# Performance work log

Measured on AMD Instinct MI355X. Metric: run time of the kernel, lower is better.

## Reference

```python
import jax, jax.numpy as jnp
import numpy as np

SINKHORN_ALPHA = 0.05
OT_MAX_ITER = 100
STOP_THR = 0.005
EPS = 1e-16
N_TOPICS, VOCAB, DIM = 1024, 50000, 256


def setup_inputs() -> dict:
    key = jax.random.key(0)
    k1, k2 = jax.random.split(key)
    x = jax.random.uniform(k1, (N_TOPICS, DIM), dtype=jnp.float32)
    y = jax.random.uniform(k2, (VOCAB, DIM), dtype=jnp.float32)
    return {"x": x, "y": y}


def _pairwise_sq_euclidean(x, y):
    return (jnp.sum(x * x, axis=1, keepdims=True)
            + jnp.sum(y * y, axis=1)
            - 2.0 * (x @ y.T))


def reference(x, y):
    M = _pairwise_sq_euclidean(x, y)          # [n, m]
    n, m = M.shape
    dt = M.dtype
    a = jnp.full((n, 1), 1.0 / n, dtype=dt)    # uniform source marginal
    b = jnp.full((m, 1), 1.0 / m, dtype=dt)    # uniform target marginal
    K = jnp.exp(-M * SINKHORN_ALPHA)           # Gibbs kernel [n, m]
    u0 = jnp.full((n, 1), 1.0 / n, dtype=dt)
    v0 = jnp.zeros((m, 1), dtype=dt)

    def cond_fn(carry):
        u, v, err, cpt = carry
        return (err > STOP_THR) & (cpt < OT_MAX_ITER)

    def body_fn(carry):
        u, v, err, cpt = carry
        v = b / (K.T @ u + EPS)                # [m, 1]
        u = a / (K @ v + EPS)                  # [n, 1]
        cpt = cpt + 1

        def compute_err(_):
            bb = v * (K.T @ u)                 # current column marginal
            return jnp.max(jnp.sum(jnp.abs(bb - b), axis=0))

        # original: convergence check only when cpt % 50 == 1
        err = jax.lax.cond((cpt % 50) == 1, compute_err, lambda _: err, operand=None)
        return (u, v, err, cpt)

    init = (u0, v0, jnp.asarray(1.0, dt), jnp.asarray(0, jnp.int32))
    u, v, err, cpt = jax.lax.while_loop(cond_fn, body_fn, init)

    transp = u * (K * v.T)                     # transport plan [n, m]
    loss_etp = jnp.sum(transp * M)
    return (loss_etp, transp)
```

## Files before the change

kernel.cpp:

```cpp
#include <hip/hip_runtime.h>
#include <hip/hip_cooperative_groups.h>
#include <cstdint>

namespace cg = cooperative_groups;

#define N_T 1024
#define M_V 50000
#define DIMS 256
#define NPAD 50048
#define GPANELS 391
#define CBLK 196
#define NPART (CBLK * 64)
#define NCHUNK 782
#define J8TOT 6250
#define F8BLK 25
#define LPART (F8BLK * 64)

constexpr float ALPHA     = 0.05f;
constexpr float INV_ALPHA = 20.0f;
constexpr float A_VAL     = 1.0f / 1024.0f;
constexpr float B_VAL     = 1.0f / 50000.0f;
constexpr float THR       = 0.005f;
constexpr float EPSV      = 1e-16f;

typedef short    bf16x8 __attribute__((ext_vector_type(8)));
typedef float    f32x4  __attribute__((ext_vector_type(4)));
typedef _Float16 half8v __attribute__((ext_vector_type(8)));

__device__ __forceinline__ float blockReduce256(float val) {
  #pragma unroll
  for (int off = 32; off; off >>= 1) val += __shfl_down(val, off, 64);
  __shared__ float redw[4];
  int lane = threadIdx.x & 63;
  int wid  = threadIdx.x >> 6;
  if (lane == 0) redw[wid] = val;
  __syncthreads();
  float r = 0.0f;
  if (threadIdx.x == 0) r = redw[0] + redw[1] + redw[2] + redw[3];
  __syncthreads();
  return r;
}

__device__ __forceinline__ unsigned short f2bf(float f) {
  union { float f; unsigned u; } c{f};
  unsigned r = c.u + 0x7FFF + ((c.u >> 16) & 1);
  return (unsigned short)(r >> 16);
}
__device__ __forceinline__ float bf2f(unsigned short b) {
  union { unsigned u; float f; } c{(unsigned)b << 16};
  return c.f;
}

__device__ __forceinline__ void gload16(const void* g, void* l) {
  __builtin_amdgcn_global_load_lds((const __attribute__((address_space(1))) unsigned int*)g,
                                   (__attribute__((address_space(3))) unsigned int*)l, 16, 0, 0);
}

__global__ __launch_bounds__(256) void pack_kernel(const float* __restrict__ x,
                                                   const float* __restrict__ y,
                                                   unsigned short* __restrict__ Ap,
                                                   unsigned short* __restrict__ Bp,
                                                   float* __restrict__ xx,
                                                   float* __restrict__ yy) {
  __shared__ float rr[4];
  int lane = threadIdx.x & 63, wid = threadIdx.x >> 6;
  if (blockIdx.x < N_T / 2) {
    int r = blockIdx.x * 2 + (threadIdx.x >> 7);
    int k = (threadIdx.x & 127) * 2;
    float2 vx = *(const float2*)&x[(size_t)r * DIMS + k];
    ushort2 h2, l2;
    h2.x = f2bf(vx.x); h2.y = f2bf(vx.y);
    l2.x = f2bf(vx.x - bf2f(h2.x)); l2.y = f2bf(vx.y - bf2f(h2.y));
    *(ushort2*)&Ap[(size_t)r * 512 + k]       = h2;
    *(ushort2*)&Ap[(size_t)r * 512 + 256 + k] = l2;
    float ssq = vx.x * vx.x + vx.y * vx.y;
    #pragma unroll
    for (int off = 32; off; off >>= 1) ssq += __shfl_down(ssq, off, 64);
    if (lane == 0) rr[wid] = ssq;
    __syncthreads();
    if ((threadIdx.x & 127) == 0) xx[r] = rr[wid] + rr[wid + 1];
  } else {
    int r = (blockIdx.x - N_T / 2) * 2 + (threadIdx.x >> 7);
    int k = (threadIdx.x & 127) * 2;
    ushort2 h2 = {0, 0};
    float ssq = 0.0f;
    if (r < M_V) {
      float2 vy = *(const float2*)&y[(size_t)r * DIMS + k];
      h2.x = f2bf(vy.x); h2.y = f2bf(vy.y);
      ssq = vy.x * vy.x + vy.y * vy.y;
    }
    *(ushort2*)&Bp[(size_t)r * 256 + k] = h2;
    #pragma unroll
    for (int off = 32; off; off >>= 1) ssq += __shfl_down(ssq, off, 64);
    if (lane == 0) rr[wid] = ssq;
    __syncthreads();
    if ((threadIdx.x & 127) == 0 && r < M_V) yy[r] = rr[wid] + rr[wid + 1];
  }
}

__global__ __launch_bounds__(256) void mfma_gemm_kernel(const unsigned short* __restrict__ Ap,
                                                        const unsigned short* __restrict__ Bp,
                                                        const float* __restrict__ xx,
                                                        const float* __restrict__ yy,
                                                        _Float16* __restrict__ Kh,
                                                        float* __restrict__ colsumPart) {
  const int t  = blockIdx.x & 63;
  const int gb = blockIdx.x >> 6;
  const int panel = gb * 8 + (t & 7);
  const int rt    = t >> 3;
  if (panel >= GPANELS) return;
  const int i0 = rt * 128;
  const int j0 = panel * 128;

  __shared__ unsigned short Ah[2][128][32];
  __shared__ unsigned short Al[2][128][32];
  __shared__ unsigned short Bs[2][128][32];
  const int tid  = threadIdx.x;
  const int lane = tid & 63;
  const int wid  = tid >> 6;
  const int wr = wid >> 1, wc = wid & 1;

  f32x4 acc[4][4];
  #pragma unroll
  for (int m = 0; m < 4; ++m)
    #pragma unroll
    for (int n = 0; n < 4; ++n) acc[m][n] = (f32x4){0.f, 0.f, 0.f, 0.f};

  const int srow  = lane >> 2;
  const int sslot = lane & 3;

  auto STAGE = [&](int b, int k0) {
    #pragma unroll
    for (int q = 0; q < 2; ++q) {
      int rbase = (wid * 2 + q) * 16;
      int row = rbase + srow;
      int cg_ = sslot ^ ((row >> 1) & 3);
      gload16(Ap + (size_t)(i0 + row) * 512 + k0 + cg_ * 8,       &Ah[b][rbase][0]);
      gload16(Ap + (size_t)(i0 + row) * 512 + 256 + k0 + cg_ * 8, &Al[b][rbase][0]);
      gload16(Bp + (size_t)(j0 + row) * 256 + k0 + cg_ * 8,       &Bs[b][rbase][0]);
    }
  };

  STAGE(0, 0);
  int cur = 0;
  #pragma unroll
  for (int step = 0; step < 8; ++step) {
    if (step < 7) {
      STAGE(cur ^ 1, (step + 1) * 32);
      asm volatile("s_waitcnt vmcnt(6)" ::: "memory");
    } else {
      asm volatile("s_waitcnt vmcnt(0)" ::: "memory");
    }
    __builtin_amdgcn_s_barrier();
    __builtin_amdgcn_sched_barrier(0);
    bf16x8 ah[4], al[4], bb[4];
    #pragma unroll
    for (int m = 0; m < 4; ++m) {
      int row = wr * 64 + m * 16 + (lane & 15);
      int sl  = (lane >> 4) ^ ((row >> 1) & 3);
      ah[m] = *(const bf16x8*)&Ah[cur][row][sl * 8];
      al[m] = *(const bf16x8*)&Al[cur][row][sl * 8];
    }
    #pragma unroll
    for (int n = 0; n < 4; ++n) {
      int col = wc * 64 + n * 16 + (lane & 15);
      int sl  = (lane >> 4) ^ ((col >> 1) & 3);
      bb[n] = *(const bf16x8*)&Bs[cur][col][sl * 8];
    }
    #pragma unroll
    for (int m = 0; m < 4; ++m)
      #pragma unroll
      for (int n = 0; n < 4; ++n) {
        acc[m][n] = __builtin_amdgcn_mfma_f32_16x16x32_bf16(ah[m], bb[n], acc[m][n], 0, 0, 0);
        acc[m][n] = __builtin_amdgcn_mfma_f32_16x16x32_bf16(al[m], bb[n], acc[m][n], 0, 0, 0);
      }
    asm volatile("s_waitcnt lgkmcnt(0)" ::: "memory");
    __builtin_amdgcn_sched_barrier(0);
    __builtin_amdgcn_s_barrier();
    cur ^= 1;
  }

  float csum[4] = {0.f, 0.f, 0.f, 0.f};
  #pragma unroll
  for (int m = 0; m < 4; ++m) {
    int rowb = i0 + wr * 64 + m * 16 + (lane >> 4) * 4;
    #pragma unroll
    for (int n = 0; n < 4; ++n) {
      int col = j0 + wc * 64 + n * 16 + (lane & 15);
      float yyc = (col < M_V) ? yy[col] : 0.0f;
      #pragma unroll
      for (int r = 0; r < 4; ++r) {
        float mval = xx[rowb + r] + yyc - 2.0f * acc[m][n][r];
        _Float16 kh = (_Float16)__expf(-ALPHA * mval);
        if (col < M_V) Kh[(size_t)(rowb + r) * M_V + col] = kh;
        csum[n] += (float)kh;
      }
    }
  }
  #pragma unroll
  for (int n = 0; n < 4; ++n) {
    float c = csum[n];
    c += __shfl_xor(c, 16, 64);
    c += __shfl_xor(c, 32, 64);
    if (lane < 16) {
      int col = j0 + wc * 64 + n * 16 + lane;
      colsumPart[(size_t)(rt * 2 + wr) * NPAD + col] = c;
    }
  }
}

__global__ __launch_bounds__(256) void v1_kernel(const float* __restrict__ cp,
                                                 float* __restrict__ v,
                                                 float* __restrict__ errAcc,
                                                 int* __restrict__ counter) {
  int j = blockIdx.x * 256 + threadIdx.x;
  if (j == 0) { errAcc[0] = 0.0f; *counter = 0; }
  if (j < M_V) {
    float s = 0.0f;
    #pragma unroll
    for (int q = 0; q < 16; ++q) s += cp[(size_t)q * NPAD + j];
    v[j] = B_VAL / (s * A_VAL + EPSV);
  }
}

__global__ __launch_bounds__(256) void rowpass_kernel(const _Float16* __restrict__ Kh,
                                                      const float* __restrict__ v,
                                                      float* __restrict__ rowPart) {
  const int i = blockIdx.y;
  const int c = blockIdx.x;
  const half8v* K8 = (const half8v*)(Kh + (size_t)i * M_V);
  const float4* v4 = (const float4*)v;
  float p = 0.0f;
  int q = c * 3125 + threadIdx.x;
  #pragma unroll
  for (int it = 0; it < 12; ++it, q += 256) {
    half8v k8 = K8[q];
    float4 va = v4[q * 2], vb = v4[q * 2 + 1];
    p += (float)k8[0] * va.x + (float)k8[1] * va.y + (float)k8[2] * va.z + (float)k8[3] * va.w
       + (float)k8[4] * vb.x + (float)k8[5] * vb.y + (float)k8[6] * vb.z + (float)k8[7] * vb.w;
  }
  if (threadIdx.x < 53) {
    int q2 = c * 3125 + 3072 + threadIdx.x;
    half8v k8 = K8[q2];
    float4 va = v4[q2 * 2], vb = v4[q2 * 2 + 1];
    p += (float)k8[0] * va.x + (float)k8[1] * va.y + (float)k8[2] * va.z + (float)k8[3] * va.w
       + (float)k8[4] * vb.x + (float)k8[5] * vb.y + (float)k8[6] * vb.z + (float)k8[7] * vb.w;
  }
  p = blockReduce256(p);
  if (threadIdx.x == 0) rowPart[c * N_T + i] = p;
}

__global__ void u_kernel(const float* __restrict__ rowPart, float* __restrict__ u) {
  int i = blockIdx.x * 256 + threadIdx.x;
  u[i] = A_VAL / (rowPart[i] + rowPart[N_T + i] + EPSV);
}

__global__ __launch_bounds__(256) void specfinal_kernel(const _Float16* __restrict__ Kh,
                                                        const float* __restrict__ u_,
                                                        const float* __restrict__ v_,
                                                        float* __restrict__ out,
                                                        float* __restrict__ sPart,
                                                        float* __restrict__ lossPart) {
  const int j8 = blockIdx.x * 256 + threadIdx.x;
  const int by = blockIdx.y;
  float contrib = 0.0f;
  if (j8 < J8TOT) {
    const size_t jb = (size_t)j8 * 8;
    float4 va = ((const float4*)v_)[j8 * 2];
    float4 vb = ((const float4*)v_)[j8 * 2 + 1];
    float sp0 = 0.f, sp1 = 0.f, sp2 = 0.f, sp3 = 0.f;
    float sp4 = 0.f, sp5 = 0.f, sp6 = 0.f, sp7 = 0.f;
    #pragma unroll
    for (int r = 0; r < 16; ++r) {
      int i = by * 16 + r;
      half8v k8 = *(const half8v*)(Kh + (size_t)i * M_V + jb);
      float ui = u_[i];
      float k0 = (float)k8[0], k1 = (float)k8[1], k2 = (float)k8[2], k3 = (float)k8[3];
      float k4 = (float)k8[4], k5 = (float)k8[5], k6 = (float)k8[6], k7 = (float)k8[7];
      float t0 = ui * k0 * va.x, t1 = ui * k1 * va.y, t2 = ui * k2 * va.z, t3 = ui * k3 * va.w;
      float t4 = ui * k4 * vb.x, t5 = ui * k5 * vb.y, t6 = ui * k6 * vb.z, t7 = ui * k7 * vb.w;
      size_t o = 1 + (size_t)i * M_V + jb;
      out[o]     = t0; out[o + 1] = t1; out[o + 2] = t2; out[o + 3] = t3;
      out[o + 4] = t4; out[o + 5] = t5; out[o + 6] = t6; out[o + 7] = t7;
      contrib += t0 * (-__logf(k0)) + t1 * (-__logf(k1)) + t2 * (-__logf(k2)) + t3 * (-__logf(k3))
               + t4 * (-__logf(k4)) + t5 * (-__logf(k5)) + t6 * (-__logf(k6)) + t7 * (-__logf(k7));
      sp0 += k0 * ui; sp1 += k1 * ui; sp2 += k2 * ui; sp3 += k3 * ui;
      sp4 += k4 * ui; sp5 += k5 * ui; sp6 += k6 * ui; sp7 += k7 * ui;
    }
    float* sb = sPart + (size_t)by * M_V + jb;
    *(float4*)sb       = make_float4(sp0, sp1, sp2, sp3);
    *(float4*)(sb + 4) = make_float4(sp4, sp5, sp6, sp7);
  }
  contrib = blockReduce256(contrib) * INV_ALPHA;
  if (threadIdx.x == 0) lossPart[by * F8BLK + blockIdx.x] = contrib;
}

__global__ __launch_bounds__(256) void tail_kernel(const float* __restrict__ sPart,
                                                   const float* __restrict__ v_,
                                                   const float* __restrict__ lossPart,
                                                   float* errAcc, int* counter,
                                                   float* out, int* notconv) {
  int j = blockIdx.x * 256 + threadIdx.x;
  float e = 0.0f;
  if (j < M_V) {
    float ss = 0.0f;
    #pragma unroll
    for (int q = 0; q < 64; ++q) ss += sPart[(size_t)q * M_V + j];
    e = fabsf(v_[j] * ss - B_VAL);
  }
  e = blockReduce256(e);
  __shared__ int lastFlag;
  if (threadIdx.x == 0) {
    atomicAdd(errAcc, e);
    __threadfence();
    int old = atomicAdd(counter, 1);
    lastFlag = (old == (int)gridDim.x - 1) ? 1 : 0;
  }
  __syncthreads();
  if (lastFlag) {
    float ls = 0.0f;
    for (int i = threadIdx.x; i < LPART; i += 256) ls += lossPart[i];
    ls = blockReduce256(ls);
    if (threadIdx.x == 0) {
      out[0] = ls;
      *notconv = (errAcc[0] > THR) ? 1 : 0;
    }
  }
}

__global__ void set1_kernel(int* p) { *p = 1; }

template <typename KT>
__global__ __launch_bounds__(256, 4) void sinkhorn_coop(const KT* Km,
                                                        float* __restrict__ u,
                                                        float* __restrict__ v,
                                                        float* __restrict__ s,
                                                        float* __restrict__ errAcc,
                                                        const int* __restrict__ notconv) {
  if (*notconv == 0) return;
  cg::grid_group grid = cg::this_grid();
  __shared__ float su[N_T];
  __shared__ float red[8][64];
  const int tid = threadIdx.x;
  const int bid = blockIdx.x;
  const int nb  = gridDim.x;
  {
    int g0 = bid * 256 + tid;
    if (g0 < N_T) u[g0] = A_VAL;
    if (g0 < 2) errAcc[g0] = 0.0f;
  }
  grid.sync();
  for (int t = 1; t <= 100; ++t) {
    const bool check = (t == 2) || (t == 52);
    for (int i = tid; i < N_T; i += 256) su[i] = u[i];
    __syncthreads();
    const int g = tid >> 5, jl = tid & 31;
    float eacc = 0.0f;
    for (int c = bid; c < NCHUNK; c += nb) {
      const int j0 = c * 64;
      const int jj = j0 + jl * 2;
      float p0 = 0.f, p1 = 0.f;
      if (jj < M_V) {
        const KT* base = Km + (size_t)(g * 128) * M_V + jj;
        #pragma unroll 4
        for (int i = 0; i < 128; ++i) {
          float k0 = (float)base[(size_t)i * M_V];
          float k1 = (float)base[(size_t)i * M_V + 1];
          float uu = su[g * 128 + i];
          p0 += k0 * uu; p1 += k1 * uu;
        }
      }
      red[g][jl * 2]     = p0;
      red[g][jl * 2 + 1] = p1;
      __syncthreads();
      if (tid < 64) {
        int j = j0 + tid;
        if (j < M_V) {
          float st = 0.f;
          #pragma unroll
          for (int q = 0; q < 8; ++q) st += red[q][tid];
          if (check) {
            s[j] = st;
            eacc += fabsf(v[j] * st - B_VAL);
          } else {
            v[j] = B_VAL / (st + EPSV);
          }
        }
      }
      __syncthreads();
    }
    if (check) {
      float e = blockReduce256(eacc);
      if (tid == 0) atomicAdd(&errAcc[t == 2 ? 0 : 1], e);
    }
    grid.sync();
    if (check) {
      float e = errAcc[t == 2 ? 0 : 1];
      if (e <= THR) break;
      if (tid < 64) {
        for (int c = bid; c < NCHUNK; c += nb) {
          int j = c * 64 + tid;
          if (j < M_V) v[j] = B_VAL / (s[j] + EPSV);
        }
      }
      grid.sync();
    }
    for (int i = bid; i < N_T; i += nb) {
      float p = 0.f;
      const KT* row = Km + (size_t)i * M_V;
      for (int j = tid; j < M_V; j += 256) p += (float)row[j] * v[j];
      p = blockReduce256(p);
      if (tid == 0) u[i] = A_VAL / (p + EPSV);
    }
    grid.sync();
  }
}

template <typename KT>
__global__ __launch_bounds__(256) void final_kernel(const KT* Kmat,
                                                    const float* __restrict__ u,
                                                    const float* __restrict__ v,
                                                    float* out,
                                                    float* __restrict__ partials,
                                                    const int* __restrict__ gate) {
  if (*gate == 0) return;
  int j = blockIdx.x * 256 + threadIdx.x;
  float contrib = 0.0f;
  if (j < M_V) {
    float vj = v[j];
    #pragma unroll 4
    for (int r = 0; r < 16; ++r) {
      int i = blockIdx.y * 16 + r;
      size_t idx = (size_t)i * M_V + j;
      float k = (float)Kmat[idx];
      float tr = u[i] * k * vj;
      float m = -__logf(k) * INV_ALPHA;
      out[1 + idx] = tr;
      contrib += tr * m;
    }
  }
  contrib = blockReduce256(contrib);
  if (threadIdx.x == 0) partials[blockIdx.y * gridDim.x + blockIdx.x] = contrib;
}

__global__ __launch_bounds__(256) void finish_kernel(const float* __restrict__ partials,
                                                     float* out, int np_,
                                                     const int* __restrict__ gate) {
  if (*gate == 0) return;
  float s = 0.0f;
  for (int i = threadIdx.x; i < np_; i += 256) s += partials[i];
  s = blockReduce256(s);
  if (threadIdx.x == 0) out[0] = s;
}

__global__ __launch_bounds__(256) void sumsq_kernel(const float* __restrict__ in,
                                                    float* __restrict__ o, int rows) {
  int r = blockIdx.x;
  if (r >= rows) return;
  float v = in[(size_t)r * DIMS + threadIdx.x];
  float s = blockReduce256(v * v);
  if (threadIdx.x == 0) o[r] = s;
}

#define BM 64
#define BN 64
#define BK 32
__global__ __launch_bounds__(256) void gemm_k_kernel(const float* __restrict__ x,
                                                     const float* __restrict__ y,
                                                     const float* __restrict__ xx,
                                                     const float* __restrict__ yy,
                                                     float* Kmat) {
  __shared__ float As[BK][BM];
  __shared__ float Bs[BK][BN + 1];
  int tid = threadIdx.x;
  int i0 = blockIdx.y * BM;
  int j0 = blockIdx.x * BN;
  int tx = tid & 15, ty = tid >> 4;
  float acc[4][4] = {};
  for (int k0 = 0; k0 < DIMS; k0 += BK) {
    #pragma unroll
    for (int l = tid; l < 512; l += 256) {
      int r = l >> 3, kq = l & 7;
      float4 a4 = *(const float4*)&x[(size_t)(i0 + r) * DIMS + k0 + kq * 4];
      As[kq * 4 + 0][r] = a4.x; As[kq * 4 + 1][r] = a4.y;
      As[kq * 4 + 2][r] = a4.z; As[kq * 4 + 3][r] = a4.w;
    }
    #pragma unroll
    for (int l = tid; l < 512; l += 256) {
      int r = l >> 3, kq = l & 7;
      int j = j0 + r;
      float4 b4 = make_float4(0.f, 0.f, 0.f, 0.f);
      if (j < M_V) b4 = *(const float4*)&y[(size_t)j * DIMS + k0 + kq * 4];
      Bs[kq * 4 + 0][r] = b4.x; Bs[kq * 4 + 1][r] = b4.y;
      Bs[kq * 4 + 2][r] = b4.z; Bs[kq * 4 + 3][r] = b4.w;
    }
    __syncthreads();
    #pragma unroll
    for (int k = 0; k < BK; ++k) {
      float a[4], b[4];
      #pragma unroll
      for (int r = 0; r < 4; ++r) a[r] = As[k][ty * 4 + r];
      #pragma unroll
      for (int c = 0; c < 4; ++c) b[c] = Bs[k][tx * 4 + c];
      #pragma unroll
      for (int r = 0; r < 4; ++r)
        #pragma unroll
        for (int c = 0; c < 4; ++c) acc[r][c] += a[r] * b[c];
    }
    __syncthreads();
  }
  #pragma unroll
  for (int r = 0; r < 4; ++r) {
    int i = i0 + ty * 4 + r;
    float xxi = xx[i];
    #pragma unroll
    for (int c = 0; c < 4; ++c) {
      int j = j0 + tx * 4 + c;
      if (j < M_V) {
        float m = xxi + yy[j] - 2.0f * acc[r][c];
        Kmat[(size_t)i * M_V + j] = __expf(-ALPHA * m);
      }
    }
  }
}

extern "C" void kernel_launch(void* const* d_in, const int* in_sizes, int n_in,
                              void* d_out, int out_size, void* d_ws, size_t ws_size,
                              hipStream_t stream) {
  const float* x = (const float*)d_in[0];
  const float* y = (const float*)d_in[1];
  float* out = (float*)d_out;

  uintptr_t wp = (uintptr_t)d_ws;
  uintptr_t wend = (uintptr_t)d_ws + ws_size;
  auto alloc = [&](size_t bytes) -> void* {
    wp = (wp + 255) & ~(uintptr_t)255;
    void* p = (void*)wp;
    wp += bytes;
    return p;
  };
  float* u        = (float*)alloc((size_t)N_T * 4);
  float* v        = (float*)alloc((size_t)M_V * 4);
  float* s        = (float*)alloc((size_t)M_V * 4);
  float* xx       = (float*)alloc((size_t)N_T * 4);
  float* yy       = (float*)alloc((size_t)M_V * 4);
  float* partials = (float*)alloc((size_t)NPART * 4);
  float* lossPart = (float*)alloc((size_t)LPART * 4);
  float* rowPart  = (float*)alloc((size_t)2 * N_T * 4);
  float* errAcc   = (float*)alloc(64);
  int*   notconv  = (int*)alloc(64);
  int*   counter  = (int*)alloc(64);
  float* colsumPart = (float*)alloc((size_t)16 * NPAD * 4);
  float* sPart    = (float*)alloc((size_t)64 * M_V * 4);

  const size_t apbytes = (size_t)N_T * 512 * 2;
  const size_t bpbytes = (size_t)NPAD * 256 * 2;
  const size_t khbytes = (size_t)N_T * M_V * 2;
  const size_t kfbytes = (size_t)N_T * M_V * 4;

  bool fast = ((wp + 1024) + apbytes + bpbytes + khbytes) <= wend;

  int dev = 0;
  hipGetDevice(&dev);
  int numCU = 256;
  hipDeviceGetAttribute(&numCU, hipDeviceAttributeMultiprocessorCount, dev);

  if (fast) {
    unsigned short* Ap = (unsigned short*)alloc(apbytes);
    unsigned short* Bp = (unsigned short*)alloc(bpbytes);
    _Float16*       Kh = (_Float16*)alloc(khbytes);

    pack_kernel<<<N_T / 2 + NPAD / 2, 256, 0, stream>>>(x, y, Ap, Bp, xx, yy);
    mfma_gemm_kernel<<<49 * 64, 256, 0, stream>>>(Ap, Bp, xx, yy, Kh, colsumPart);

    v1_kernel<<<CBLK, 256, 0, stream>>>(colsumPart, v, errAcc, counter);
    rowpass_kernel<<<dim3(2, N_T), 256, 0, stream>>>(Kh, v, rowPart);
    u_kernel<<<N_T / 256, 256, 0, stream>>>(rowPart, u);
    specfinal_kernel<<<dim3(F8BLK, 64), 256, 0, stream>>>(Kh, u, v, out, sPart, lossPart);
    tail_kernel<<<CBLK, 256, 0, stream>>>(sPart, v, lossPart, errAcc, counter, out, notconv);

    int occS = 0;
    hipOccupancyMaxActiveBlocksPerMultiprocessor(&occS, sinkhorn_coop<_Float16>, 256, 0);
    long sCap = (long)occS * numCU;
    int sGrid = (int)(sCap < 1024 ? sCap : 1024);
    if (sGrid < 1) sGrid = 1;
    void* coopArgs[] = {(void*)&Kh, (void*)&u, (void*)&v, (void*)&s,
                        (void*)&errAcc, (void*)&notconv};
    hipLaunchCooperativeKernel(reinterpret_cast<void*>(sinkhorn_coop<_Float16>),
                               dim3(sGrid), dim3(256), coopArgs, 0, stream);
    final_kernel<_Float16><<<dim3(CBLK, 64), 256, 0, stream>>>(Kh, u, v, out, partials, notconv);
    finish_kernel<<<1, 256, 0, stream>>>(partials, out, NPART, notconv);
  } else {
    sumsq_kernel<<<N_T, 256, 0, stream>>>(x, xx, N_T);
    sumsq_kernel<<<M_V, 256, 0, stream>>>(y, yy, M_V);
    bool k_in_ws = ((wp + 512) + kfbytes) <= wend;
    float* Kmat = k_in_ws ? (float*)alloc(kfbytes) : out + 1;
    gemm_k_kernel<<<dim3((M_V + BN - 1) / BN, N_T / BM), 256, 0, stream>>>(x, y, xx, yy, Kmat);
    set1_kernel<<<1, 1, 0, stream>>>(notconv);
    int occS = 0;
    hipOccupancyMaxActiveBlocksPerMultiprocessor(&occS, sinkhorn_coop<float>, 256, 0);
    long sCap = (long)occS * numCU;
    int sGrid = (int)(sCap < 1024 ? sCap : 1024);
    if (sGrid < 1) sGrid = 1;
    void* coopArgs[] = {(void*)&Kmat, (void*)&u, (void*)&v, (void*)&s,
                        (void*)&errAcc, (void*)&notconv};
    hipLaunchCooperativeKernel(reinterpret_cast<void*>(sinkhorn_coop<float>),
                               dim3(sGrid), dim3(256), coopArgs, 0, stream);
    final_kernel<float><<<dim3(CBLK, 64), 256, 0, stream>>>(Kmat, u, v, out, partials, notconv);
    finish_kernel<<<1, 256, 0, stream>>>(partials, out, NPART, notconv);
  }
}
```

Baseline: 261.1 us.

## Single-buffer A tiles in GEMM, add occupancy bound, fuse u into rowpass

The GEMM kernel keeps only one LDS buffer for the A (hi/lo) tiles and double-buffers B, so LDS use drops. A is reloaded after a barrier that follows the fragment reads, and __launch_bounds__(256,4) asks for higher occupancy. Separately, rowpass now lets one block reduce a whole row and write u directly, which removes the u_kernel launch and the rowPart buffer. The risks are an extra barrier per k-step, a more serialized A load, and half as many rowpass blocks.

```diff
diff --git a/kernel.cpp b/kernel.cpp
--- a/kernel.cpp
+++ b/kernel.cpp
@@ -98,12 +98,12 @@
   }
 }
 
-__global__ __launch_bounds__(256) void mfma_gemm_kernel(const unsigned short* __restrict__ Ap,
-                                                        const unsigned short* __restrict__ Bp,
-                                                        const float* __restrict__ xx,
-                                                        const float* __restrict__ yy,
-                                                        _Float16* __restrict__ Kh,
-                                                        float* __restrict__ colsumPart) {
+__global__ __launch_bounds__(256, 4) void mfma_gemm_kernel(const unsigned short* __restrict__ Ap,
+                                                           const unsigned short* __restrict__ Bp,
+                                                           const float* __restrict__ xx,
+                                                           const float* __restrict__ yy,
+                                                           _Float16* __restrict__ Kh,
+                                                           float* __restrict__ colsumPart) {
   const int t  = blockIdx.x & 63;
   const int gb = blockIdx.x >> 6;
   const int panel = gb * 8 + (t & 7);
@@ -112,8 +112,8 @@
   const int i0 = rt * 128;
   const int j0 = panel * 128;
 
-  __shared__ unsigned short Ah[2][128][32];
-  __shared__ unsigned short Al[2][128][32];
+  __shared__ unsigned short Ah[128][32];
+  __shared__ unsigned short Al[128][32];
   __shared__ unsigned short Bs[2][128][32];
   const int tid  = threadIdx.x;
   const int lane = tid & 63;
@@ -129,25 +129,34 @@
   const int srow  = lane >> 2;
   const int sslot = lane & 3;
 
-  auto STAGE = [&](int b, int k0) {
+  auto STAGE_A = [&](int k0) {
     #pragma unroll
     for (int q = 0; q < 2; ++q) {
       int rbase = (wid * 2 + q) * 16;
       int row = rbase + srow;
       int cg_ = sslot ^ ((row >> 1) & 3);
-      gload16(Ap + (size_t)(i0 + row) * 512 + k0 + cg_ * 8,       &Ah[b][rbase][0]);
-      gload16(Ap + (size_t)(i0 + row) * 512 + 256 + k0 + cg_ * 8, &Al[b][rbase][0]);
-      gload16(Bp + (size_t)(j0 + row) * 256 + k0 + cg_ * 8,       &Bs[b][rbase][0]);
+      gload16(Ap + (size_t)(i0 + row) * 512 + k0 + cg_ * 8,       &Ah[rbase][0]);
+      gload16(Ap + (size_t)(i0 + row) * 512 + 256 + k0 + cg_ * 8, &Al[rbase][0]);
     }
   };
-
-  STAGE(0, 0);
+  auto STAGE_B = [&](int b, int k0) {
+    #pragma unroll
+    for (int q = 0; q < 2; ++q) {
+      int rbase = (wid * 2 + q) * 16;
+      int row = rbase + srow;
+      int cg_ = sslot ^ ((row >> 1) & 3);
+      gload16(Bp + (size_t)(j0 + row) * 256 + k0 + cg_ * 8, &Bs[b][rbase][0]);
+    }
+  };
+
+  STAGE_A(0);
+  STAGE_B(0, 0);
   int cur = 0;
   #pragma unroll
   for (int step = 0; step < 8; ++step) {
     if (step < 7) {
-      STAGE(cur ^ 1, (step + 1) * 32);
-      asm volatile("s_waitcnt vmcnt(6)" ::: "memory");
+      STAGE_B(cur ^ 1, (step + 1) * 32);
+      asm volatile("s_waitcnt vmcnt(2)" ::: "memory");
     } else {
       asm volatile("s_waitcnt vmcnt(0)" ::: "memory");
     }
@@ -158,8 +167,8 @@
     for (int m = 0; m < 4; ++m) {
       int row = wr * 64 + m * 16 + (lane & 15);
       int sl  = (lane >> 4) ^ ((row >> 1) & 3);
-      ah[m] = *(const bf16x8*)&Ah[cur][row][sl * 8];
-      al[m] = *(const bf16x8*)&Al[cur][row][sl * 8];
+      ah[m] = *(const bf16x8*)&Ah[row][sl * 8];
+      al[m] = *(const bf16x8*)&Al[row][sl * 8];
     }
     #pragma unroll
     for (int n = 0; n < 4; ++n) {
@@ -167,6 +176,10 @@
       int sl  = (lane >> 4) ^ ((col >> 1) & 3);
       bb[n] = *(const bf16x8*)&Bs[cur][col][sl * 8];
     }
+    asm volatile("s_waitcnt lgkmcnt(0)" ::: "memory");
+    __builtin_amdgcn_sched_barrier(0);
+    __builtin_amdgcn_s_barrier();
+    if (step < 7) STAGE_A((step + 1) * 32);
     #pragma unroll
     for (int m = 0; m < 4; ++m)
       #pragma unroll
@@ -174,9 +187,6 @@
         acc[m][n] = __builtin_amdgcn_mfma_f32_16x16x32_bf16(ah[m], bb[n], acc[m][n], 0, 0, 0);
         acc[m][n] = __builtin_amdgcn_mfma_f32_16x16x32_bf16(al[m], bb[n], acc[m][n], 0, 0, 0);
       }
-    asm volatile("s_waitcnt lgkmcnt(0)" ::: "memory");
-    __builtin_amdgcn_sched_barrier(0);
-    __builtin_amdgcn_s_barrier();
     cur ^= 1;
   }
 
@@ -225,34 +235,28 @@
 
 __global__ __launch_bounds__(256) void rowpass_kernel(const _Float16* __restrict__ Kh,
                                                       const float* __restrict__ v,
-                                                      float* __restrict__ rowPart) {
-  const int i = blockIdx.y;
-  const int c = blockIdx.x;
+                                                      float* __restrict__ u) {
+  const int i = blockIdx.x;
   const half8v* K8 = (const half8v*)(Kh + (size_t)i * M_V);
   const float4* v4 = (const float4*)v;
   float p = 0.0f;
-  int q = c * 3125 + threadIdx.x;
+  int q = threadIdx.x;
   #pragma unroll
-  for (int it = 0; it < 12; ++it, q += 256) {
+  for (int it = 0; it < 24; ++it, q += 256) {
     half8v k8 = K8[q];
     float4 va = v4[q * 2], vb = v4[q * 2 + 1];
     p += (float)k8[0] * va.x + (float)k8[1] * va.y + (float)k8[2] * va.z + (float)k8[3] * va.w
        + (float)k8[4] * vb.x + (float)k8[5] * vb.y + (float)k8[6] * vb.z + (float)k8[7] * vb.w;
   }
-  if (threadIdx.x < 53) {
-    int q2 = c * 3125 + 3072 + threadIdx.x;
+  if (threadIdx.x < 106) {
+    int q2 = 6144 + threadIdx.x;
     half8v k8 = K8[q2];
     float4 va = v4[q2 * 2], vb = v4[q2 * 2 + 1];
     p += (float)k8[0] * va.x + (float)k8[1] * va.y + (float)k8[2] * va.z + (float)k8[3] * va.w
        + (float)k8[4] * vb.x + (float)k8[5] * vb.y + (float)k8[6] * vb.z + (float)k8[7] * vb.w;
   }
   p = blockReduce256(p);
-  if (threadIdx.x == 0) rowPart[c * N_T + i] = p;
-}
-
-__global__ void u_kernel(const float* __restrict__ rowPart, float* __restrict__ u) {
-  int i = blockIdx.x * 256 + threadIdx.x;
-  u[i] = A_VAL / (rowPart[i] + rowPart[N_T + i] + EPSV);
+  if (threadIdx.x == 0) u[i] = A_VAL / (p + EPSV);
 }
 
 __global__ __launch_bounds__(256) void specfinal_kernel(const _Float16* __restrict__ Kh,
@@ -546,7 +550,6 @@
   float* yy       = (float*)alloc((size_t)M_V * 4);
   float* partials = (float*)alloc((size_t)NPART * 4);
   float* lossPart = (float*)alloc((size_t)LPART * 4);
-  float* rowPart  = (float*)alloc((size_t)2 * N_T * 4);
   float* errAcc   = (float*)alloc(64);
   int*   notconv  = (int*)alloc(64);
   int*   counter  = (int*)alloc(64);
@@ -574,8 +577,7 @@
     mfma_gemm_kernel<<<49 * 64, 256, 0, stream>>>(Ap, Bp, xx, yy, Kh, colsumPart);
 
     v1_kernel<<<CBLK, 256, 0, stream>>>(colsumPart, v, errAcc, counter);
-    rowpass_kernel<<<dim3(2, N_T), 256, 0, stream>>>(Kh, v, rowPart);
-    u_kernel<<<N_T / 256, 256, 0, stream>>>(rowPart, u);
+    rowpass_kernel<<<N_T, 256, 0, stream>>>(Kh, v, u);
     specfinal_kernel<<<dim3(F8BLK, 64), 256, 0, stream>>>(Kh, u, v, out, sPart, lossPart);
     tail_kernel<<<CBLK, 256, 0, stream>>>(sPart, v, lossPart, errAcc, counter, out, notconv);
 
```

Measured after the change: 305.4 us. 17.0% more time.
